# Kernel tuning notes

Measured on AMD Instinct MI355X. Metric: run time of the kernel, lower is better.

The kernel has to match this reference:

```python
import jax, jax.numpy as jnp
import numpy as np

B = 1048576
N_BINS = 64
LOGIT_SCALE = 10.0  # cur_logit_scale default, detached in the original


def setup_inputs() -> dict:
    key = jax.random.key(0)
    k1, k2, k3 = jax.random.split(key, 3)
    y_hat = jax.random.normal(k1, (B, N_BINS), dtype=jnp.float32)
    t = jax.random.randint(k2, (B,), 0, N_BINS, dtype=jnp.int64)
    e = jax.random.randint(k3, (B,), 0, 2, dtype=jnp.int64)
    return {"y_hat": y_hat, "t": t, "e": e}


def reference(y_hat, t, e):
    # SurvEMD forward: p=2, raw_distance=True, reduction='mean'
    n_bins = y_hat.shape[-1]
    dt = y_hat.dtype
    t = t.reshape(-1, 1)
    e = e.reshape(-1, 1).astype(dt)  # binary censoring indicator as float
    j = jnp.arange(n_bins)  # bin index vector

    # convert_survival_label, vectorized:
    # target[i,j] = 1 at j==t[i]; plus (1-e[i]) for all j > t[i]
    onehot = (j == t).astype(dt)
    target = onehot + (1.0 - e) * (j > t).astype(dt)  # values in {0,1}

    target_dist = jax.nn.softmax((2.0 * target - 1.0) * LOGIT_SCALE, axis=-1)
    pred = (1.0 - e) * ((1.0 - target) * y_hat + target * LOGIT_SCALE) + e * y_hat
    pred_dist = jax.nn.softmax(pred, axis=-1)

    # cdf_loss with p=2, normalize_dist=False, ret_raw=True:
    d = jnp.cumsum(pred_dist, axis=-1) - jnp.cumsum(target_dist, axis=-1)
    loss = jnp.sum(d * d, axis=-1)  # [B]
    return loss.mean()
```

## Files before the change

kernel.cpp:

```cpp
#include <hip/hip_runtime.h>

#define NBINS 64

__global__ __launch_bounds__(256) void survemd_kernel(
    const float* __restrict__ y_hat,
    const int* __restrict__ t,
    const int* __restrict__ e,
    float* __restrict__ out,
    int n_rows)
{
    const int lane = threadIdx.x & 63;
    const int wave_in_block = threadIdx.x >> 6;
    const int waves_per_block = blockDim.x >> 6;
    const int wave_id = blockIdx.x * waves_per_block + wave_in_block;
    const int total_waves = gridDim.x * waves_per_block;

    const float s = 2.0611536224385579e-9f;
    float acc = 0.0f;

    for (int row = wave_id; row < n_rows; row += total_waves) {
        const int urow = __builtin_amdgcn_readfirstlane(row);
        const int tt = t[urow];
        const int ee = e[urow];

        const float y = y_hat[(size_t)urow * NBINS + lane];

        const bool ge = (lane >= tt);
        const float pred = (ee == 0 && ge) ? 10.0f : y;
        float x = __expf(pred);

        #pragma unroll
        for (int off = 1; off < 64; off <<= 1) {
            float v = __shfl_up(x, off, 64);
            if (lane >= off) x += v;
        }
        const float total = __shfl(x, 63, 64);
        const float cps = x * __builtin_amdgcn_rcpf(total);

        const float k = (ee == 1) ? 1.0f : (float)(NBINS - tt);
        const float rden = __builtin_amdgcn_rcpf(k + (64.0f - k) * s);
        const float hi = rden;
        const float lo = s * rden;
        const float ones = ge ? ((ee == 1) ? 1.0f : (float)(lane - tt + 1)) : 0.0f;
        const float cts = ones * hi + ((float)(lane + 1) - ones) * lo;

        const float d = cps - cts;
        acc = fmaf(d, d, acc);
    }

    #pragma unroll
    for (int off = 32; off >= 1; off >>= 1)
        acc += __shfl_down(acc, off, 64);

    __shared__ float wave_sums[8];
    if (lane == 0) wave_sums[wave_in_block] = acc;
    __syncthreads();
    if (threadIdx.x == 0) {
        float bsum = 0.0f;
        for (int w = 0; w < waves_per_block; ++w) bsum += wave_sums[w];
        atomicAdd(out, bsum * (1.0f / (float)n_rows));
    }
}

extern "C" void kernel_launch(void* const* d_in, const int* in_sizes, int n_in,
                              void* d_out, int out_size, void* d_ws, size_t ws_size,
                              hipStream_t stream) {
    const float* y_hat = (const float*)d_in[0];
    const int*   t     = (const int*)d_in[1];
    const int*   e     = (const int*)d_in[2];
    float* out = (float*)d_out;

    const int n_rows = in_sizes[1];

    hipMemsetAsync(out, 0, out_size * sizeof(float), stream);

    const int block = 256;
    const int grid  = 8192;
    survemd_kernel<<<grid, block, 0, stream>>>(y_hat, t, e, out, n_rows);
}
```

Measured before the change: 440.0 us.

## Process four rows per wave with float4 loads and DPP segmented scan

Each wave now handles four rows at once. Every 16-lane segment loads one row as float4, so each lane covers four bins. The prefix sum is done within each lane first, then across the 16-lane segment with DPP row-shift adds in place of the 64-lane shuffle scan, and the loop is unrolled to process two quads per iteration. This aims to cut cross-lane shuffle latency and per-row overhead and to widen memory accesses, at the cost of more registers per lane and a per-lane t/e load instead of a scalar one.

```diff
diff --git a/kernel.cpp b/kernel.cpp
--- a/kernel.cpp
+++ b/kernel.cpp
@@ -1,6 +1,71 @@
 #include <hip/hip_runtime.h>
 
 #define NBINS 64
+
+template <int CTRL>
+__device__ __forceinline__ float dpp_shr_add(float x) {
+    int xi = __float_as_int(x);
+    int sh = __builtin_amdgcn_update_dpp(0, xi, CTRL, 0xF, 0xF, true);
+    return x + __int_as_float(sh);
+}
+
+__device__ __forceinline__ float quad_rows(const float4* __restrict__ yv,
+                                           const int* __restrict__ t,
+                                           const int* __restrict__ e,
+                                           int quad, int lane, int n_rows) {
+    const int seg = lane >> 4;
+    const int sl  = lane & 15;
+    const int row = quad * 4 + seg;
+    const bool valid = row < n_rows;
+    const int crow = valid ? row : (n_rows - 1);
+
+    const int tt = t[crow];
+    const int ee = e[crow];
+    const float4 y = yv[(size_t)crow * (NBINS / 4) + sl];
+
+    const int j0 = sl * 4;
+
+    const bool cen = (ee == 0);
+    const float x0 = __expf((cen && (j0 + 0 >= tt)) ? 10.0f : y.x);
+    const float x1 = __expf((cen && (j0 + 1 >= tt)) ? 10.0f : y.y);
+    const float x2 = __expf((cen && (j0 + 2 >= tt)) ? 10.0f : y.z);
+    const float x3 = __expf((cen && (j0 + 3 >= tt)) ? 10.0f : y.w);
+
+    const float p0 = x0;
+    const float p1 = p0 + x1;
+    const float p2 = p1 + x2;
+    const float p3 = p2 + x3;
+
+    float sc = p3;
+    sc = dpp_shr_add<0x111>(sc);
+    sc = dpp_shr_add<0x112>(sc);
+    sc = dpp_shr_add<0x114>(sc);
+    sc = dpp_shr_add<0x118>(sc);
+
+    const float total = __shfl(sc, 15, 16);
+    const float excl  = sc - p3;
+    const float rtot  = __builtin_amdgcn_rcpf(total);
+    const float er    = excl * rtot;
+
+    const float s = 2.0611536224385579e-9f;
+    const float k  = (ee == 1) ? 1.0f : (float)(NBINS - tt);
+    const float hi = __builtin_amdgcn_rcpf(k + (64.0f - k) * s);
+    const float lo = s * hi;
+
+    float acc = 0.0f;
+    #pragma unroll
+    for (int c = 0; c < 4; ++c) {
+        const int j = j0 + c;
+        const float p = (c == 0) ? p0 : (c == 1) ? p1 : (c == 2) ? p2 : p3;
+        const float ones = (j >= tt) ? ((ee == 1) ? 1.0f : (float)(j - tt + 1))
+                                     : 0.0f;
+        const float cts = ones * hi + ((float)(j + 1) - ones) * lo;
+        const float cps = fmaf(p, rtot, er);
+        const float d = cps - cts;
+        acc = fmaf(d, d, acc);
+    }
+    return valid ? acc : 0.0f;
+}
 
 __global__ __launch_bounds__(256) void survemd_kernel(
     const float* __restrict__ y_hat,
@@ -15,37 +80,15 @@
     const int wave_id = blockIdx.x * waves_per_block + wave_in_block;
     const int total_waves = gridDim.x * waves_per_block;
 
-    const float s = 2.0611536224385579e-9f;
+    const float4* yv = (const float4*)y_hat;
+    const int nquads = (n_rows + 3) >> 2;
+
     float acc = 0.0f;
-
-    for (int row = wave_id; row < n_rows; row += total_waves) {
-        const int urow = __builtin_amdgcn_readfirstlane(row);
-        const int tt = t[urow];
-        const int ee = e[urow];
-
-        const float y = y_hat[(size_t)urow * NBINS + lane];
-
-        const bool ge = (lane >= tt);
-        const float pred = (ee == 0 && ge) ? 10.0f : y;
-        float x = __expf(pred);
-
-        #pragma unroll
-        for (int off = 1; off < 64; off <<= 1) {
-            float v = __shfl_up(x, off, 64);
-            if (lane >= off) x += v;
-        }
-        const float total = __shfl(x, 63, 64);
-        const float cps = x * __builtin_amdgcn_rcpf(total);
-
-        const float k = (ee == 1) ? 1.0f : (float)(NBINS - tt);
-        const float rden = __builtin_amdgcn_rcpf(k + (64.0f - k) * s);
-        const float hi = rden;
-        const float lo = s * rden;
-        const float ones = ge ? ((ee == 1) ? 1.0f : (float)(lane - tt + 1)) : 0.0f;
-        const float cts = ones * hi + ((float)(lane + 1) - ones) * lo;
-
-        const float d = cps - cts;
-        acc = fmaf(d, d, acc);
+    for (int q = wave_id; q < nquads; q += 2 * total_waves) {
+        acc += quad_rows(yv, t, e, q, lane, n_rows);
+        const int q2 = q + total_waves;
+        if (q2 < nquads)
+            acc += quad_rows(yv, t, e, q2, lane, n_rows);
     }
 
     #pragma unroll
@@ -72,7 +115,7 @@
 
     const int n_rows = in_sizes[1];
 
-    hipMemsetAsync(out, 0, out_size * sizeof(float), stream);
+    (void)hipMemsetAsync(out, 0, out_size * sizeof(float), stream);
 
     const int block = 256;
     const int grid  = 8192;
```

After: 405.8 us. 1.08x faster.

## Process 16 rows per wave with float4 loads, serial scans and DPP combine

Applied to the files above, without the earlier changes.

Each wave now handles 16 rows at a time. Every lane loads four float4 vectors covering 16 bins of one row and runs a serial 16-element prefix sum in registers, then combines lane partials across each quad with DPP permutes instead of a 6-step wave-wide shuffle scan. Rows are split into contiguous per-wave chunks, the next group is prefetched into registers while the current one is computed, and the grid shrinks to 2048 blocks with a launch-bounds occupancy hint. The per-bin target CDF is rewritten as a linear slope/offset form. The aim is wider memory transactions and less cross-lane work, at the cost of higher register pressure.

```diff
diff --git a/kernel.cpp b/kernel.cpp
--- a/kernel.cpp
+++ b/kernel.cpp
@@ -2,7 +2,90 @@
 
 #define NBINS 64
 
-__global__ __launch_bounds__(256) void survemd_kernel(
+template <int CTRL>
+__device__ __forceinline__ float qperm(float x) {
+    return __int_as_float(__builtin_amdgcn_update_dpp(
+        0, __float_as_int(x), CTRL, 0xF, 0xF, true));
+}
+
+struct Group {
+    float4 y[4];
+    int    t, e;
+};
+
+__device__ __forceinline__ void load_group(Group& g,
+                                           const float4* __restrict__ yv,
+                                           const int* __restrict__ t,
+                                           const int* __restrict__ e,
+                                           int grp, int lane, int n_rows) {
+    const size_t base = (size_t)grp * (16 * NBINS / 4) + lane * 4;
+    #pragma unroll
+    for (int c = 0; c < 4; ++c) g.y[c] = yv[base + c];
+    const int row = grp * 16 + (lane >> 2);
+    const int crow = min(row, n_rows - 1);
+    g.t = t[crow];
+    g.e = e[crow];
+}
+
+__device__ __forceinline__ float compute_group(const Group& g, int grp,
+                                               int lane, float m1, float m2,
+                                               float m3, int n_rows) {
+    const int li = lane & 3;
+    const int j0 = li * 16;
+    const int tt = g.t;
+    const int ee = g.e;
+    const bool cen = (ee == 0);
+    const float E10 = 22026.465794806718f;
+
+    float p[16];
+    #pragma unroll
+    for (int c = 0; c < 4; ++c) {
+        const float4 y = g.y[c];
+        #pragma unroll
+        for (int k = 0; k < 4; ++k) {
+            const int idx = c * 4 + k;
+            const float yy = (k == 0) ? y.x : (k == 1) ? y.y
+                           : (k == 2) ? y.z : y.w;
+            const float ex = __expf(yy);
+            const bool force = cen && (j0 + idx >= tt);
+            p[idx] = force ? E10 : ex;
+        }
+    }
+    #pragma unroll
+    for (int idx = 1; idx < 16; ++idx) p[idx] += p[idx - 1];
+    const float L = p[15];
+
+    const float b0 = qperm<0x00>(L);
+    const float b1 = qperm<0x55>(L);
+    const float b2 = qperm<0xAA>(L);
+    const float b3 = qperm<0xFF>(L);
+    const float excl  = fmaf(m1, b0, fmaf(m2, b1, m3 * b2));
+    const float total = (b0 + b1) + (b2 + b3);
+    const float rtot  = __builtin_amdgcn_rcpf(total);
+    const float er    = excl * rtot;
+
+    const float s = 2.0611536224385579e-9f;
+    const float k  = (ee == 1) ? 1.0f : (float)(NBINS - tt);
+    const float hi = __builtin_amdgcn_rcpf(k + (64.0f - k) * s);
+    const float lo = s * hi;
+    const float hl = hi - lo;
+    const float slope = cen ? hl : 0.0f;
+    const float off   = cen ? (float)(1 - tt) * hl : hl;
+
+    float acc = 0.0f;
+    #pragma unroll
+    for (int idx = 0; idx < 16; ++idx) {
+        const int j = j0 + idx;
+        const float m   = (j >= tt) ? fmaf((float)j, slope, off) : 0.0f;
+        const float cts = fmaf((float)(j + 1), lo, m);
+        const float d   = fmaf(p[idx], rtot, er - cts);
+        acc = fmaf(d, d, acc);
+    }
+    const int row = grp * 16 + (lane >> 2);
+    return (row < n_rows) ? acc : 0.0f;
+}
+
+__global__ __launch_bounds__(256, 4) void survemd_kernel(
     const float* __restrict__ y_hat,
     const int* __restrict__ t,
     const int* __restrict__ e,
@@ -15,37 +98,28 @@
     const int wave_id = blockIdx.x * waves_per_block + wave_in_block;
     const int total_waves = gridDim.x * waves_per_block;
 
-    const float s = 2.0611536224385579e-9f;
+    const float4* yv = (const float4*)y_hat;
+    const int li = lane & 3;
+    const float m1 = (li >= 1) ? 1.0f : 0.0f;
+    const float m2 = (li >= 2) ? 1.0f : 0.0f;
+    const float m3 = (li >= 3) ? 1.0f : 0.0f;
+
+    const int ngroups = (n_rows + 15) >> 4;
+    const int gpw     = (ngroups + total_waves - 1) / total_waves;
+    const int begin   = wave_id * gpw;
+    const int end     = min(begin + gpw, ngroups);
+
     float acc = 0.0f;
-
-    for (int row = wave_id; row < n_rows; row += total_waves) {
-        const int urow = __builtin_amdgcn_readfirstlane(row);
-        const int tt = t[urow];
-        const int ee = e[urow];
-
-        const float y = y_hat[(size_t)urow * NBINS + lane];
-
-        const bool ge = (lane >= tt);
-        const float pred = (ee == 0 && ge) ? 10.0f : y;
-        float x = __expf(pred);
-
-        #pragma unroll
-        for (int off = 1; off < 64; off <<= 1) {
-            float v = __shfl_up(x, off, 64);
-            if (lane >= off) x += v;
+    if (begin < end) {
+        Group A;
+        load_group(A, yv, t, e, begin, lane, n_rows);
+        for (int i = begin; i < end; ++i) {
+            Group B;
+            const int nxt = (i + 1 < end) ? i + 1 : i;
+            load_group(B, yv, t, e, nxt, lane, n_rows);
+            acc += compute_group(A, i, lane, m1, m2, m3, n_rows);
+            A = B;
         }
-        const float total = __shfl(x, 63, 64);
-        const float cps = x * __builtin_amdgcn_rcpf(total);
-
-        const float k = (ee == 1) ? 1.0f : (float)(NBINS - tt);
-        const float rden = __builtin_amdgcn_rcpf(k + (64.0f - k) * s);
-        const float hi = rden;
-        const float lo = s * rden;
-        const float ones = ge ? ((ee == 1) ? 1.0f : (float)(lane - tt + 1)) : 0.0f;
-        const float cts = ones * hi + ((float)(lane + 1) - ones) * lo;
-
-        const float d = cps - cts;
-        acc = fmaf(d, d, acc);
     }
 
     #pragma unroll
@@ -72,9 +146,9 @@
 
     const int n_rows = in_sizes[1];
 
-    hipMemsetAsync(out, 0, out_size * sizeof(float), stream);
+    (void)hipMemsetAsync(out, 0, out_size * sizeof(float), stream);
 
     const int block = 256;
-    const int grid  = 8192;
+    const int grid  = 2048;
     survemd_kernel<<<grid, block, 0, stream>>>(y_hat, t, e, out, n_rows);
 }
```

After: 363.4 us. -17.4%, faster.
